# Kernel optimization log

Measured on AMD Instinct MI355X. Metric: run time of the kernel, lower is better.

## Reference

```python
import jax, jax.numpy as jnp
import numpy as np

CARDS = [1000000, 500000, 100000, 50000, 10000, 10000, 5000, 5000, 1000, 1000,
         500, 500, 100, 100, 50, 50, 20, 20, 10, 10, 5, 5, 3, 3, 2, 2]

def _emb_dim(card):
    return int(min(32, max(4, round(1.6 * card ** 0.56))))

DIMS = [_emb_dim(c) for c in CARDS]          # per-table embedding dims (torch rule)
ROWS = [c + 1 for c in CARDS]                # +1 for UNK row at index 0 (padding_idx)
OFFS = np.concatenate([[0], np.cumsum(ROWS)[:-1]]).astype(np.int64)
TOTAL_ROWS = int(sum(ROWS))
MAX_D = 32
NUM_CONT = 64
B = 131072
CAT_DIM = int(sum(DIMS))                     # 508
FUSED_IN = CAT_DIM + 32                      # cont MLP outputs 32
LN_EPS = 1e-5


def setup_inputs() -> dict:
    key = jax.random.key(0)
    ks = jax.random.split(key, 10)
    x_cont = jax.random.normal(ks[0], (B, NUM_CONT), dtype=jnp.float32)
    # per-column indices in [0, card_i] (0 = UNK/padding)
    cols = [jax.random.randint(jax.random.fold_in(ks[1], i), (B,), 0, r, dtype=jnp.int64)
            for i, r in enumerate(ROWS)]
    x_cat = jnp.stack(cols, axis=1)  # [B, 26] int64
    # all tables stacked into one flat [TOTAL_ROWS, 32] array; table i uses cols [:DIMS[i]]
    emb_flat = jax.random.normal(ks[2], (TOTAL_ROWS, MAX_D), dtype=jnp.float32) * 0.05
    emb_flat = emb_flat.at[np.asarray(OFFS)].set(0.0)  # padding_idx=0 rows are zero
    # cont MLP: Linear(64,32) + LayerNorm(32) + SiLU
    Wc = jax.random.normal(ks[3], (NUM_CONT, 32), dtype=jnp.float32) * (1.0 / np.sqrt(NUM_CONT))
    bc = jnp.zeros((32,), jnp.float32)
    ln_g = jnp.ones((32,), jnp.float32)
    ln_b = jnp.zeros((32,), jnp.float32)
    # proj: Linear(540,64)+SiLU, Linear(64,32)+SiLU (dropout = identity in eval)
    W1 = jax.random.normal(ks[4], (FUSED_IN, 64), dtype=jnp.float32) * (1.0 / np.sqrt(FUSED_IN))
    b1 = jnp.zeros((64,), jnp.float32)
    W2 = jax.random.normal(ks[5], (64, 32), dtype=jnp.float32) * (1.0 / np.sqrt(64))
    b2 = jnp.zeros((32,), jnp.float32)
    return {"x_cont": x_cont, "x_cat": x_cat, "emb_flat": emb_flat,
            "Wc": Wc, "bc": bc, "ln_g": ln_g, "ln_b": ln_b,
            "W1": W1, "b1": b1, "W2": W2, "b2": b2}


def reference(x_cont, x_cat, emb_flat, Wc, bc, ln_g, ln_b, W1, b1, W2, b2):
    # --- multi-table embedding gather + concat (eval: dropout = identity) ---
    gidx = x_cat + jnp.asarray(OFFS)[None, :]          # [B, T] global row ids
    rows = emb_flat[gidx]                               # [B, T, 32] single fused gather
    rows = rows * (x_cat != 0).astype(rows.dtype)[..., None]  # padding_idx semantics
    cat = jnp.concatenate([rows[:, i, :d] for i, d in enumerate(DIMS)], axis=1)  # [B, 508]
    # --- cont MLP: Linear + LayerNorm + SiLU ---
    h = x_cont @ Wc + bc                                # [B, 32]
    mu = jnp.mean(h, axis=-1, keepdims=True)
    var = jnp.var(h, axis=-1, keepdims=True)
    h = (h - mu) / jnp.sqrt(var + LN_EPS) * ln_g + ln_b
    h = jax.nn.silu(h)
    # --- fuse + proj MLP ---
    fused = jnp.concatenate([h, cat], axis=1)           # [B, 540]
    z = jax.nn.silu(fused @ W1 + b1)                    # [B, 64]
    z = jax.nn.silu(z @ W2 + b2)                        # [B, 32]
    return z
```

## Files before the change

kernel.cpp:

```cpp
#include <hip/hip_runtime.h>

typedef __attribute__((ext_vector_type(8))) short bf16x8;
typedef __attribute__((ext_vector_type(4))) float f32x4;

#define NT 26
#define BROWS 32
#define NKS 18
#define LDSTR 584
#define Z1STR 68
#define WS_FRAG_DWORDS 18432

__constant__ int4 c_TAB[NT] = {
    {0,32,8,0},{1000001,64,8,0},{1500002,96,8,0},{1600003,128,8,0},
    {1650004,160,8,0},{1660005,192,8,0},{1670006,224,8,0},{1675007,256,8,0},
    {1680008,288,8,0},{1681009,320,8,0},{1682010,352,8,0},{1682511,384,8,0},
    {1683012,416,6,0},{1683113,440,6,0},{1683214,464,4,0},{1683265,480,4,0},
    {1683316,496,3,0},{1683337,508,3,0},{1683358,520,2,0},{1683369,528,2,0},
    {1683380,536,1,0},{1683386,540,1,0},{1683392,544,1,0},{1683396,548,1,0},
    {1683400,552,1,0},{1683403,556,1,0}};

__constant__ int c_P_COLP[NT] = {
    0,32,64,96,128,160,192,224,256,288,320,352,384,408,432,448,464,476,
    488,496,504,508,512,516,520,524};
__constant__ int c_P_DIMS[NT] = {
    32,32,32,32,32,32,32,32,32,32,32,32,21,21,14,14,9,9,6,6,4,4,4,4,4,4};
__constant__ int c_P_COLF[NT] = {
    0,32,64,96,128,160,192,224,256,288,320,352,384,405,426,440,454,463,
    472,478,484,488,492,496,500,504};

__device__ __forceinline__ unsigned short f2bf(float f) {
  unsigned int u = __builtin_bit_cast(unsigned int, f);
  u += 0x7fffu + ((u >> 16) & 1u);
  return (unsigned short)(u >> 16);
}

__device__ __forceinline__ unsigned cvtpk(float a, float b) {
  unsigned r;
  asm("v_cvt_pk_bf16_f32 %0, %1, %2" : "=v"(r) : "v"(a), "v"(b));
  return r;
}

__device__ __forceinline__ uint4 pk4(float4 a, float4 b) {
  uint4 o;
  o.x = cvtpk(a.x, a.y); o.y = cvtpk(a.z, a.w);
  o.z = cvtpk(b.x, b.y); o.w = cvtpk(b.z, b.w);
  return o;
}

__device__ __forceinline__ uint2 pk2(float4 a) {
  uint2 o;
  o.x = cvtpk(a.x, a.y); o.y = cvtpk(a.z, a.w);
  return o;
}

__device__ __forceinline__ float silu_f(float x) {
  return x / (1.0f + __expf(-x));
}

extern "C" __global__ void __launch_bounds__(256)
prep_w1(const float* __restrict__ W1, unsigned int* __restrict__ wsf) {
  const int g = blockIdx.x * 256 + threadIdx.x;
  if (g >= WS_FRAG_DWORDS) return;
  const int f  = g * 2;
  const int j  = f & 7;
  const int l  = (f >> 3) & 63;
  const int w  = (f >> 9) & 3;
  const int ks = f >> 11;
  const int bn = (w << 4) + (l & 15);
  const int k0 = (ks << 5) + ((l >> 4) << 3) + j;
  float v[2];
  #pragma unroll
  for (int e = 0; e < 2; ++e) {
    const int k = k0 + e;
    float x = 0.0f;
    if (k < 32) {
      x = W1[k * 64 + bn];
    } else {
      const int c = k - 32;
      for (int i = 0; i < NT; ++i) {
        const int off = c - c_P_COLP[i];
        if (off >= 0 && off < c_P_DIMS[i])
          x = W1[(32 + c_P_COLF[i] + off) * 64 + bn];
      }
    }
    v[e] = x;
  }
  wsf[g] = ((unsigned)f2bf(v[0])) | (((unsigned)f2bf(v[1])) << 16);
}

extern "C" __global__ void __launch_bounds__(256, 2)
tab_fused(const float* __restrict__ xc,
          const int* __restrict__ xcat,
          const float* __restrict__ emb,
          const float* __restrict__ Wc,
          const float* __restrict__ bc,
          const float* __restrict__ lng,
          const float* __restrict__ lnb,
          const unsigned short* __restrict__ wsf,
          const float* __restrict__ b1,
          const float* __restrict__ W2,
          const float* __restrict__ b2,
          float* __restrict__ out) {
  __shared__ __attribute__((aligned(16))) float smem[(BROWS * LDSTR) / 2];
  unsigned short* fused = (unsigned short*)smem;
  float* z1 = smem;

  const int t  = threadIdx.x;
  const int w  = t >> 6;
  const int l  = t & 63;
  const int R0 = blockIdx.x * BROWS;

  const int bn = (w << 4) + (l & 15);
  const int kg = (l >> 4) << 3;

  const int r_ = t & 31;
  const int i0 = t >> 5;
  const bool has3 = (t < 64);
  const int i3 = 24 + (t >> 5);
  const int* xrow = xcat + (size_t)(R0 + r_) * NT;
  const int idx0 = xrow[i0];
  const int idx1 = xrow[i0 + 8];
  const int idx2 = xrow[i0 + 16];
  const int idx3 = has3 ? xrow[i3] : 0;

  const int4 tb0 = c_TAB[i0];
  const int4 tb1 = c_TAB[i0 + 8];
  const int4 tb2 = c_TAB[i0 + 16];
  const int4 tb3 = c_TAB[has3 ? i3 : 24];

  const float4* s0 = (const float4*)(emb + (size_t)(tb0.x + idx0) * 32);
  const float4* s1 = (const float4*)(emb + (size_t)(tb1.x + idx1) * 32);
  const float4* s2 = (const float4*)(emb + (size_t)(tb2.x + idx2) * 32);
  const float4* s3 = (const float4*)(emb + (size_t)(tb3.x + idx3) * 32);

  const float4 A0 = s0[0], A1 = s0[1], A2 = s0[2], A3 = s0[3];
  const float4 A4 = s0[4], A5 = s0[5], A6 = s0[6], A7 = s0[7];
  const float4 B0 = s1[0], B1 = s1[1], B2 = s1[2], B3 = s1[3];
  const float4 B4 = s1[4], B5 = s1[5], B6 = s1[6], B7 = s1[7];
  const float4 C0 = s2[0], C1 = s2[1], C2 = s2[2];
  float4 D0;
  if (has3) D0 = s3[0];

  if (t < 64) {
    uint4 zz = {0u, 0u, 0u, 0u};
    *(uint4*)((char*)fused + (t >> 1) * (LDSTR * 2) + (560 + (t & 1) * 8) * 2) = zz;
  }

  char* rowb = (char*)fused + r_ * (LDSTR * 2);
  {
    uint4* d4 = (uint4*)(rowb + tb0.y * 2);
    d4[0] = pk4(A0, A1); d4[1] = pk4(A2, A3);
    d4[2] = pk4(A4, A5); d4[3] = pk4(A6, A7);
  }
  {
    uint4* d4 = (uint4*)(rowb + tb1.y * 2);
    d4[0] = pk4(B0, B1); d4[1] = pk4(B2, B3);
    if (tb1.z >= 6) d4[2] = pk4(B4, B5);
    if (tb1.z == 8) d4[3] = pk4(B6, B7);
  }
  {
    uint2* d2 = (uint2*)(rowb + tb2.y * 2);
    d2[0] = pk2(C0);
    if (tb2.z >= 2) d2[1] = pk2(C1);
    if (tb2.z == 3) d2[2] = pk2(C2);
  }
  if (has3) {
    uint2* d2 = (uint2*)(rowb + tb3.y * 2);
    d2[0] = pk2(D0);
  }

  {
    const int r  = t >> 3;
    const int j0 = (t & 7) << 2;
    const float* xr = xc + (size_t)(R0 + r) * 64;
    float h0 = bc[j0], h1 = bc[j0 + 1], h2 = bc[j0 + 2], h3 = bc[j0 + 3];
    #pragma unroll 4
    for (int k4 = 0; k4 < 16; ++k4) {
      const float4 x4 = ((const float4*)xr)[k4];
      const float* wb = Wc + (k4 * 4) * 32 + j0;
      const float4 w0 = *(const float4*)(wb);
      const float4 w1 = *(const float4*)(wb + 32);
      const float4 w2 = *(const float4*)(wb + 64);
      const float4 w3 = *(const float4*)(wb + 96);
      h0 = __fmaf_rn(x4.x, w0.x, h0); h1 = __fmaf_rn(x4.x, w0.y, h1);
      h2 = __fmaf_rn(x4.x, w0.z, h2); h3 = __fmaf_rn(x4.x, w0.w, h3);
      h0 = __fmaf_rn(x4.y, w1.x, h0); h1 = __fmaf_rn(x4.y, w1.y, h1);
      h2 = __fmaf_rn(x4.y, w1.z, h2); h3 = __fmaf_rn(x4.y, w1.w, h3);
      h0 = __fmaf_rn(x4.z, w2.x, h0); h1 = __fmaf_rn(x4.z, w2.y, h1);
      h2 = __fmaf_rn(x4.z, w2.z, h2); h3 = __fmaf_rn(x4.z, w2.w, h3);
      h0 = __fmaf_rn(x4.w, w3.x, h0); h1 = __fmaf_rn(x4.w, w3.y, h1);
      h2 = __fmaf_rn(x4.w, w3.z, h2); h3 = __fmaf_rn(x4.w, w3.w, h3);
    }
    float s1v = h0 + h1 + h2 + h3;
    float s2v = h0 * h0 + h1 * h1 + h2 * h2 + h3 * h3;
    #pragma unroll
    for (int m = 1; m < 8; m <<= 1) {
      s1v += __shfl_xor(s1v, m);
      s2v += __shfl_xor(s2v, m);
    }
    const float mu = s1v * 0.03125f;
    const float var = s2v * 0.03125f - mu * mu;
    const float rs = rsqrtf(var + 1e-5f);
    const float g0 = silu_f((h0 - mu) * rs * lng[j0]     + lnb[j0]);
    const float g1 = silu_f((h1 - mu) * rs * lng[j0 + 1] + lnb[j0 + 1]);
    const float g2 = silu_f((h2 - mu) * rs * lng[j0 + 2] + lnb[j0 + 2]);
    const float g3 = silu_f((h3 - mu) * rs * lng[j0 + 3] + lnb[j0 + 3]);
    uint2 hw;
    hw.x = cvtpk(g0, g1);
    hw.y = cvtpk(g2, g3);
    *(uint2*)((char*)fused + r * (LDSTR * 2) + j0 * 2) = hw;
  }

  bf16x8 bfw[NKS];
  #pragma unroll
  for (int ks = 0; ks < NKS; ++ks)
    bfw[ks] = *(const bf16x8*)(wsf + ((ks * 4 + w) * 64 + l) * 8);
  __syncthreads();

  f32x4 acc[2];
  acc[0] = (f32x4){0.f, 0.f, 0.f, 0.f};
  acc[1] = (f32x4){0.f, 0.f, 0.f, 0.f};
  const unsigned short* arow0 = &fused[(l & 15) * LDSTR + kg];
  const unsigned short* arow1 = arow0 + 16 * LDSTR;
  #pragma unroll
  for (int ks = 0; ks < NKS; ++ks) {
    acc[0] = __builtin_amdgcn_mfma_f32_16x16x32_bf16(
        *(const bf16x8*)(arow0 + (ks << 5)), bfw[ks], acc[0], 0, 0, 0);
    acc[1] = __builtin_amdgcn_mfma_f32_16x16x32_bf16(
        *(const bf16x8*)(arow1 + (ks << 5)), bfw[ks], acc[1], 0, 0, 0);
  }
  __syncthreads();

  {
    const float b1v = b1[bn];
    const int rb = (l >> 4) << 2;
    #pragma unroll
    for (int mt = 0; mt < 2; ++mt) {
      #pragma unroll
      for (int v = 0; v < 4; ++v) {
        const int row = (mt << 4) + rb + v;
        z1[row * Z1STR + bn] = silu_f(acc[mt][v] + b1v);
      }
    }
  }
  __syncthreads();

  {
    const int r  = t >> 3;
    const int j0 = (t & 7) << 2;
    float a0 = b2[j0], a1 = b2[j0 + 1], a2 = b2[j0 + 2], a3 = b2[j0 + 3];
    const float4* zr4 = (const float4*)&z1[r * Z1STR];
    #pragma unroll
    for (int k4 = 0; k4 < 16; ++k4) {
      const float4 zv = zr4[k4];
      const float* w2b = W2 + (k4 * 4) * 32 + j0;
      const float4 w0 = *(const float4*)(w2b);
      const float4 w1 = *(const float4*)(w2b + 32);
      const float4 w2v = *(const float4*)(w2b + 64);
      const float4 w3 = *(const float4*)(w2b + 96);
      a0 = __fmaf_rn(zv.x, w0.x, a0); a1 = __fmaf_rn(zv.x, w0.y, a1);
      a2 = __fmaf_rn(zv.x, w0.z, a2); a3 = __fmaf_rn(zv.x, w0.w, a3);
      a0 = __fmaf_rn(zv.y, w1.x, a0); a1 = __fmaf_rn(zv.y, w1.y, a1);
      a2 = __fmaf_rn(zv.y, w1.z, a2); a3 = __fmaf_rn(zv.y, w1.w, a3);
      a0 = __fmaf_rn(zv.z, w2v.x, a0); a1 = __fmaf_rn(zv.z, w2v.y, a1);
      a2 = __fmaf_rn(zv.z, w2v.z, a2); a3 = __fmaf_rn(zv.z, w2v.w, a3);
      a0 = __fmaf_rn(zv.w, w3.x, a0); a1 = __fmaf_rn(zv.w, w3.y, a1);
      a2 = __fmaf_rn(zv.w, w3.z, a2); a3 = __fmaf_rn(zv.w, w3.w, a3);
    }
    float4 o;
    o.x = silu_f(a0); o.y = silu_f(a1); o.z = silu_f(a2); o.w = silu_f(a3);
    *(float4*)(out + (size_t)(R0 + r) * 32 + j0) = o;
  }
}

extern "C" void kernel_launch(void* const* d_in, const int* in_sizes, int n_in,
                              void* d_out, int out_size, void* d_ws, size_t ws_size,
                              hipStream_t stream) {
  const float* xc   = (const float*)d_in[0];
  const int*   xcat = (const int*)  d_in[1];
  const float* emb  = (const float*)d_in[2];
  const float* Wc   = (const float*)d_in[3];
  const float* bc   = (const float*)d_in[4];
  const float* lng  = (const float*)d_in[5];
  const float* lnb  = (const float*)d_in[6];
  const float* W1   = (const float*)d_in[7];
  const float* b1   = (const float*)d_in[8];
  const float* W2   = (const float*)d_in[9];
  const float* b2   = (const float*)d_in[10];
  float* out = (float*)d_out;

  unsigned int* wsf = (unsigned int*)d_ws;
  hipLaunchKernelGGL(prep_w1, dim3((WS_FRAG_DWORDS + 255) / 256), dim3(256),
                     0, stream, W1, wsf);

  const int B = in_sizes[0] / 64;
  const int grid = B / BROWS;
  hipLaunchKernelGGL(tab_fused, dim3(grid), dim3(256), 0, stream,
                     xc, xcat, emb, Wc, bc, lng, lnb,
                     (const unsigned short*)wsf, b1, W2, b2, out);
}
```

Measured before the change: 125.9 us.

## Stage categorical indices in LDS and coalesce embedding gathers across lanes

The kernel first copies the block's categorical indices into shared memory. The embedding gather is then reorganised so that groups of lanes each read contiguous 16-byte slices of one embedding row, replacing the old scheme where each thread fetched whole rows serially. Tables now get padded column slots, which widens the fused row to 616 and adds a 19th K-step to the MFMA loop. The goal is better memory coalescing and more loads in flight on the gather. The cost is an extra barrier, more LDS, and extra MFMA work on the padding columns.

```diff
diff --git a/kernel.cpp b/kernel.cpp
--- a/kernel.cpp
+++ b/kernel.cpp
@@ -5,23 +5,19 @@
 
 #define NT 26
 #define BROWS 32
-#define NKS 18
-#define LDSTR 584
+#define NKS 19
+#define LDSTR 616
 #define Z1STR 68
-#define WS_FRAG_DWORDS 18432
-
-__constant__ int4 c_TAB[NT] = {
-    {0,32,8,0},{1000001,64,8,0},{1500002,96,8,0},{1600003,128,8,0},
-    {1650004,160,8,0},{1660005,192,8,0},{1670006,224,8,0},{1675007,256,8,0},
-    {1680008,288,8,0},{1681009,320,8,0},{1682010,352,8,0},{1682511,384,8,0},
-    {1683012,416,6,0},{1683113,440,6,0},{1683214,464,4,0},{1683265,480,4,0},
-    {1683316,496,3,0},{1683337,508,3,0},{1683358,520,2,0},{1683369,528,2,0},
-    {1683380,536,1,0},{1683386,540,1,0},{1683392,544,1,0},{1683396,548,1,0},
-    {1683400,552,1,0},{1683403,556,1,0}};
+#define WS_FRAG_DWORDS 19456
+
+__constant__ int c_OFFS[NT] = {
+    0,1000001,1500002,1600003,1650004,1660005,1670006,1675007,1680008,1681009,
+    1682010,1682511,1683012,1683113,1683214,1683265,1683316,1683337,1683358,
+    1683369,1683380,1683386,1683392,1683396,1683400,1683403};
 
 __constant__ int c_P_COLP[NT] = {
-    0,32,64,96,128,160,192,224,256,288,320,352,384,408,432,448,464,476,
-    488,496,504,508,512,516,520,524};
+    0,32,64,96,128,160,192,224,256,288,320,352,384,416,448,464,480,496,
+    512,520,528,532,536,540,544,548};
 __constant__ int c_P_DIMS[NT] = {
     32,32,32,32,32,32,32,32,32,32,32,32,21,21,14,14,9,9,6,6,4,4,4,4,4,4};
 __constant__ int c_P_COLF[NT] = {
@@ -38,13 +34,6 @@
   unsigned r;
   asm("v_cvt_pk_bf16_f32 %0, %1, %2" : "=v"(r) : "v"(a), "v"(b));
   return r;
-}
-
-__device__ __forceinline__ uint4 pk4(float4 a, float4 b) {
-  uint4 o;
-  o.x = cvtpk(a.x, a.y); o.y = cvtpk(a.z, a.w);
-  o.z = cvtpk(b.x, b.y); o.w = cvtpk(b.z, b.w);
-  return o;
 }
 
 __device__ __forceinline__ uint2 pk2(float4 a) {
@@ -102,7 +91,9 @@
           const float* __restrict__ b2,
           float* __restrict__ out) {
   __shared__ __attribute__((aligned(16))) float smem[(BROWS * LDSTR) / 2];
+  __shared__ __attribute__((aligned(16))) int xs[BROWS * NT];
   unsigned short* fused = (unsigned short*)smem;
+  char* tbb = (char*)smem;
   float* z1 = smem;
 
   const int t  = threadIdx.x;
@@ -113,60 +104,47 @@
   const int bn = (w << 4) + (l & 15);
   const int kg = (l >> 4) << 3;
 
-  const int r_ = t & 31;
-  const int i0 = t >> 5;
-  const bool has3 = (t < 64);
-  const int i3 = 24 + (t >> 5);
-  const int* xrow = xcat + (size_t)(R0 + r_) * NT;
-  const int idx0 = xrow[i0];
-  const int idx1 = xrow[i0 + 8];
-  const int idx2 = xrow[i0 + 16];
-  const int idx3 = has3 ? xrow[i3] : 0;
-
-  const int4 tb0 = c_TAB[i0];
-  const int4 tb1 = c_TAB[i0 + 8];
-  const int4 tb2 = c_TAB[i0 + 16];
-  const int4 tb3 = c_TAB[has3 ? i3 : 24];
-
-  const float4* s0 = (const float4*)(emb + (size_t)(tb0.x + idx0) * 32);
-  const float4* s1 = (const float4*)(emb + (size_t)(tb1.x + idx1) * 32);
-  const float4* s2 = (const float4*)(emb + (size_t)(tb2.x + idx2) * 32);
-  const float4* s3 = (const float4*)(emb + (size_t)(tb3.x + idx3) * 32);
-
-  const float4 A0 = s0[0], A1 = s0[1], A2 = s0[2], A3 = s0[3];
-  const float4 A4 = s0[4], A5 = s0[5], A6 = s0[6], A7 = s0[7];
-  const float4 B0 = s1[0], B1 = s1[1], B2 = s1[2], B3 = s1[3];
-  const float4 B4 = s1[4], B5 = s1[5], B6 = s1[6], B7 = s1[7];
-  const float4 C0 = s2[0], C1 = s2[1], C2 = s2[2];
-  float4 D0;
-  if (has3) D0 = s3[0];
-
-  if (t < 64) {
+  if (t < 208) ((int4*)xs)[t] = ((const int4*)(xcat + (size_t)R0 * NT))[t];
+  if (t >= 160) {
+    const int tt = t - 160;
     uint4 zz = {0u, 0u, 0u, 0u};
-    *(uint4*)((char*)fused + (t >> 1) * (LDSTR * 2) + (560 + (t & 1) * 8) * 2) = zz;
-  }
-
-  char* rowb = (char*)fused + r_ * (LDSTR * 2);
-  {
-    uint4* d4 = (uint4*)(rowb + tb0.y * 2);
-    d4[0] = pk4(A0, A1); d4[1] = pk4(A2, A3);
-    d4[2] = pk4(A4, A5); d4[3] = pk4(A6, A7);
-  }
-  {
-    uint4* d4 = (uint4*)(rowb + tb1.y * 2);
-    d4[0] = pk4(B0, B1); d4[1] = pk4(B2, B3);
-    if (tb1.z >= 6) d4[2] = pk4(B4, B5);
-    if (tb1.z == 8) d4[3] = pk4(B6, B7);
-  }
-  {
-    uint2* d2 = (uint2*)(rowb + tb2.y * 2);
-    d2[0] = pk2(C0);
-    if (tb2.z >= 2) d2[1] = pk2(C1);
-    if (tb2.z == 3) d2[2] = pk2(C2);
-  }
-  if (has3) {
-    uint2* d2 = (uint2*)(rowb + tb3.y * 2);
-    d2[0] = pk2(D0);
+    *(uint4*)(tbb + (tt / 3) * (LDSTR * 2) + 1168 + (tt % 3) * 16) = zz;
+  }
+  __syncthreads();
+
+  const int rowA = (w << 3) + (l >> 3);
+  const int qA = l & 7;
+  float4 vA[14];
+  #pragma unroll
+  for (int u = 0; u < 14; ++u) {
+    const int idx = xs[rowA * NT + u];
+    vA[u] = *(const float4*)(emb + ((size_t)(c_OFFS[u] + idx) << 5) + (qA << 2));
+  }
+  const int pbb = (w << 4) + (l >> 2);
+  const int rowB = pbb & 31;
+  const int qB = l & 3;
+  float4 vB[2];
+  #pragma unroll
+  for (int u = 0; u < 2; ++u) {
+    const int tab = 14 + (u << 1) + (pbb >> 5);
+    const int idx = xs[rowB * NT + tab];
+    vB[u] = *(const float4*)(emb + ((size_t)(c_OFFS[tab] + idx) << 5) + (qB << 2));
+  }
+  const bool hasC = (w < 2);
+  const int rowC = l >> 1, qC = l & 1, tabC = 18 + w;
+  float4 vC = {0.f, 0.f, 0.f, 0.f};
+  if (hasC) {
+    const int idx = xs[rowC * NT + tabC];
+    vC = *(const float4*)(emb + ((size_t)(c_OFFS[tabC] + idx) << 5) + (qC << 2));
+  }
+  const bool hasD = (w != 1);
+  const int dD = (w == 2) ? 0 : ((w == 3) ? 1 : 2);
+  const int tabD = 20 + (dD << 1) + (l >> 5);
+  const int rowD = l & 31;
+  float4 vD = {0.f, 0.f, 0.f, 0.f};
+  if (hasD) {
+    const int idx = xs[rowD * NT + tabD];
+    vD = *(const float4*)(emb + ((size_t)(c_OFFS[tabD] + idx) << 5));
   }
 
   {
@@ -208,7 +186,21 @@
     uint2 hw;
     hw.x = cvtpk(g0, g1);
     hw.y = cvtpk(g2, g3);
-    *(uint2*)((char*)fused + r * (LDSTR * 2) + j0 * 2) = hw;
+    *(uint2*)(tbb + r * (LDSTR * 2) + j0 * 2) = hw;
+  }
+
+  {
+    char* dA = tbb + rowA * (LDSTR * 2) + 64 + qA * 8;
+    #pragma unroll
+    for (int u = 0; u < 14; ++u) *(uint2*)(dA + u * 64) = pk2(vA[u]);
+    char* dB = tbb + rowB * (LDSTR * 2) + 960 + (pbb >> 5) * 32 + qB * 8;
+    #pragma unroll
+    for (int u = 0; u < 2; ++u) *(uint2*)(dB + u * 64) = pk2(vB[u]);
+    if (hasC)
+      *(uint2*)(tbb + rowC * (LDSTR * 2) + 1088 + w * 16 + qC * 8) = pk2(vC);
+    if (hasD)
+      *(uint2*)(tbb + rowD * (LDSTR * 2) + 1120 +
+                (((dD << 1) + (l >> 5)) << 3)) = pk2(vD);
   }
 
   bf16x8 bfw[NKS];
```

Result: faster. 112.8 us (-10.5%).
